# Kernel tuning notes

Measured on AMD Instinct MI355X. Metric: run time of the kernel, lower is better.

Reference implementation:

```python
import jax, jax.numpy as jnp
import numpy as np

INPUT_DIM = 6
HIDDEN = 256
NUM_CLASSES = 8
B = 16
V = 32768


def setup_inputs() -> dict:
    key = jax.random.key(0)
    ks = jax.random.split(key, 8)
    x = jax.random.normal(ks[0], (B, INPUT_DIM, V), dtype=jnp.float32)
    obj_idx = jax.random.randint(ks[1], (B,), 0, NUM_CLASSES)
    # Stacked per-class expert weights (Conv1d kernel_size=1 == pointwise linear)
    s1 = 1.0 / np.sqrt(INPUT_DIM)
    s2 = 1.0 / np.sqrt(HIDDEN)
    w1 = jax.random.uniform(ks[2], (NUM_CLASSES, HIDDEN, INPUT_DIM), jnp.float32, -s1, s1)
    b1 = jax.random.uniform(ks[3], (NUM_CLASSES, HIDDEN), jnp.float32, -s1, s1)
    w2 = jax.random.uniform(ks[4], (NUM_CLASSES, HIDDEN, HIDDEN), jnp.float32, -s2, s2)
    b2 = jax.random.uniform(ks[5], (NUM_CLASSES, HIDDEN), jnp.float32, -s2, s2)
    w3 = jax.random.uniform(ks[6], (NUM_CLASSES, 1, HIDDEN), jnp.float32, -s2, s2)
    b3 = jax.random.uniform(ks[7], (NUM_CLASSES, 1), jnp.float32, -s2, s2)
    return {"x": x, "obj_idx": obj_idx, "w1": w1, "b1": b1,
            "w2": w2, "b2": b2, "w3": w3, "b3": b3}


def reference(x, obj_idx, w1, b1, w2, b2, w3, b3):
    # Gather each sample's expert weights, then run the fused 3-layer pointwise
    # MLP over all B*V positions in one batched einsum per layer (no Python
    # loop over samples, unlike the original torch code).
    # x: [B, 6, V] -> out: [B, 1, V]
    h = jax.nn.relu(jnp.einsum('boi,biv->bov', w1[obj_idx], x) + b1[obj_idx][:, :, None])
    h = jax.nn.relu(jnp.einsum('boi,biv->bov', w2[obj_idx], h) + b2[obj_idx][:, :, None])
    out = jnp.einsum('boi,biv->bov', w3[obj_idx], h) + b3[obj_idx][:, :, None]
    return out
```

## Files before the change

kernel.cpp:

```cpp
#include <hip/hip_runtime.h>
#include <hip/hip_bf16.h>

typedef __bf16 bf16x8 __attribute__((ext_vector_type(8)));
typedef __bf16 bf16x4 __attribute__((ext_vector_type(4)));
typedef float  f32x4  __attribute__((ext_vector_type(4)));

#define V_TOTAL 32768
#define NT      512
#define NV      32
#define NBLK    256

#define W2_LDS  114688
#define H1_LDS  32768
#define RED_LDS 4096
#define LDS_TOT (W2_LDS + H1_LDS + RED_LDS)

#define GLOAD_LDS16(g, l) __builtin_amdgcn_global_load_lds( \
    (const __attribute__((address_space(1))) void*)(g),     \
    (__attribute__((address_space(3))) void*)(l), 16, 0, 0)

__global__ void w2_to_bf16(const float* __restrict__ w2, __bf16* __restrict__ w2b) {
    int i = blockIdx.x * 256 + threadIdx.x;
    int e = i >> 16, q = i & 65535, c = q >> 3, j = q & 7;
    int kt = c >> 10, mt16 = (c >> 6) & 15, ko = (c >> 4) & 3, row = c & 15;
    w2b[i] = (__bf16)w2[e * 65536 + (mt16 * 16 + row) * 256 + kt * 32 + ko * 8 + j];
}

__global__ __launch_bounds__(NT) void fused_mlp(
    const float* __restrict__ x,  const int* __restrict__ obj,
    const float* __restrict__ w1, const float* __restrict__ b1,
    const float* __restrict__ b2, const float* __restrict__ w3,
    const float* __restrict__ b3, const __bf16* __restrict__ w2b,
    float* __restrict__ out)
{
    extern __shared__ __align__(16) char smem[];
    char*  w2s = smem;
    char*  h1t = smem + W2_LDS;
    float* red = (float*)(smem + W2_LDS + H1_LDS);

    const int t    = threadIdx.x;
    const int lane = t & 63;
    const int wv   = t >> 6;
    const int llo  = lane & 15;
    const int lhi  = lane >> 4;
    const int b    = blockIdx.x >> 4;
    const int g    = blockIdx.x & 15;
    const int e    = __builtin_amdgcn_readfirstlane(obj[b]);
    const __bf16* w2sw = w2b + (size_t)e * 65536;

    #pragma unroll
    for (int it = 0; it < 14; ++it) {
        int c0 = it * NT + wv * 64;
        GLOAD_LDS16(w2sw + c0 * 8 + lane * 8, w2s + c0 * 16);
    }

    bf16x8 aa7[2];
    #pragma unroll
    for (int mt = 0; mt < 2; ++mt) {
        int c = 7168 + (2 * wv + mt) * 64 + lane;
        aa7[mt] = *(const bf16x8*)(w2sw + c * 8);
    }

    const float* w1e = w1 + e * 1536;
    bf16x8 aa1[2];
    f32x4  b1f[2], bv[2], wf[2];
    #pragma unroll
    for (int mt2 = 0; mt2 < 2; ++mt2) {
        const int m0 = (2 * wv + mt2) * 16;
        bf16x8 v = {};
        if (lhi == 0)
            #pragma unroll
            for (int j = 0; j < 6; ++j) v[j] = (__bf16)w1e[(m0 + llo) * 6 + j];
        aa1[mt2] = v;
        b1f[mt2] = *(const f32x4*)(b1 + e * 256 + m0 + lhi * 4);
        bv[mt2]  = *(const f32x4*)(b2 + e * 256 + m0 + lhi * 4);
        wf[mt2]  = *(const f32x4*)(w3 + e * 256 + m0 + lhi * 4);
    }
    const float b3e = b3[e];
    const float* xe = x + (size_t)b * 6 * V_TOTAL;

    bf16x8 xf[4];
    #pragma unroll
    for (int pt = 0; pt < 4; ++pt) {
        bf16x8 v = {};
        #pragma unroll
        for (int i = 0; i < 6; ++i)
            v[i] = (__bf16)xe[i * V_TOTAL + g * (NV * 64) + pt * 16 + llo];
        xf[pt] = v;
    }

    for (int iv = 0; iv < NV; ++iv) {
        const int v0 = (g * NV + iv) * 64;

        #pragma unroll
        for (int mt2 = 0; mt2 < 2; ++mt2) {
            const int o = (2 * wv + mt2) * 2 + (lhi >> 1);
            char* wbase = h1t + (o >> 2) * 4096 + (o & 3) * 256
                              + llo * 16 + (lhi & 1) * 8;
            #pragma unroll
            for (int pt = 0; pt < 4; ++pt) {
                f32x4 h = __builtin_amdgcn_mfma_f32_16x16x32_bf16(
                    aa1[mt2], xf[pt], b1f[mt2], 0, 0, 0);
                bf16x4 pk;
                #pragma unroll
                for (int r = 0; r < 4; ++r) pk[r] = (__bf16)fmaxf(h[r], 0.f);
                *(bf16x4*)(wbase + pt * 1024) = pk;
            }
        }
        if (iv + 1 < NV)
            #pragma unroll
            for (int pt = 0; pt < 4; ++pt) {
                bf16x8 v = {};
                #pragma unroll
                for (int i = 0; i < 6; ++i)
                    v[i] = (__bf16)xe[i * V_TOTAL + v0 + 64 + pt * 16 + llo];
                xf[pt] = v;
            }
        __syncthreads();

        f32x4 acc[2][4];
        #pragma unroll
        for (int mt = 0; mt < 2; ++mt)
            #pragma unroll
            for (int nt = 0; nt < 4; ++nt) acc[mt][nt] = bv[mt];
        const char* abase = w2s + wv * 2048 + lane * 16;
        const char* bbase = h1t + lane * 16;
        __builtin_amdgcn_s_setprio(1);
        #pragma unroll
        for (int kt = 0; kt < 7; ++kt) {
            bf16x8 bb[4];
            #pragma unroll
            for (int nt = 0; nt < 4; ++nt)
                bb[nt] = *(const bf16x8*)(bbase + kt * 4096 + nt * 1024);
            #pragma unroll
            for (int mt = 0; mt < 2; ++mt) {
                const bf16x8 aw = *(const bf16x8*)(abase + kt * 16384 + mt * 1024);
                #pragma unroll
                for (int nt = 0; nt < 4; ++nt)
                    acc[mt][nt] = __builtin_amdgcn_mfma_f32_16x16x32_bf16(
                        aw, bb[nt], acc[mt][nt], 0, 0, 0);
            }
        }
        {
            bf16x8 bb[4];
            #pragma unroll
            for (int nt = 0; nt < 4; ++nt)
                bb[nt] = *(const bf16x8*)(bbase + 7 * 4096 + nt * 1024);
            #pragma unroll
            for (int mt = 0; mt < 2; ++mt)
                #pragma unroll
                for (int nt = 0; nt < 4; ++nt)
                    acc[mt][nt] = __builtin_amdgcn_mfma_f32_16x16x32_bf16(
                        aa7[mt], bb[nt], acc[mt][nt], 0, 0, 0);
        }
        __builtin_amdgcn_s_setprio(0);

        float p[4];
        #pragma unroll
        for (int nt = 0; nt < 4; ++nt) {
            float s = 0.f;
            #pragma unroll
            for (int mt = 0; mt < 2; ++mt)
                #pragma unroll
                for (int j = 0; j < 4; ++j)
                    s = fmaf(wf[mt][j], fmaxf(acc[mt][nt][j], 0.f), s);
            s += __shfl_xor(s, 16, 64);
            s += __shfl_xor(s, 32, 64);
            p[nt] = s;
        }
        float* rp = red + (iv & 1) * 512;
        if (lane < 16)
            #pragma unroll
            for (int nt = 0; nt < 4; ++nt)
                rp[wv * 64 + nt * 16 + lane] = p[nt];
        __syncthreads();
        if (t < 64) {
            float s = b3e;
            #pragma unroll
            for (int w8 = 0; w8 < 8; ++w8) s += rp[w8 * 64 + t];
            out[(size_t)b * V_TOTAL + v0 + t] = s;
        }
    }
}

extern "C" void kernel_launch(void* const* d_in, const int* in_sizes, int n_in,
                              void* d_out, int out_size, void* d_ws, size_t ws_size,
                              hipStream_t stream) {
    const float* x   = (const float*)d_in[0];
    const int*   obj = (const int*)d_in[1];
    const float* w1  = (const float*)d_in[2];
    const float* b1  = (const float*)d_in[3];
    const float* w2  = (const float*)d_in[4];
    const float* b2  = (const float*)d_in[5];
    const float* w3  = (const float*)d_in[6];
    const float* b3  = (const float*)d_in[7];
    float*  out = (float*)d_out;
    __bf16* w2b = (__bf16*)d_ws;

    (void)hipFuncSetAttribute((const void*)fused_mlp,
                              hipFuncAttributeMaxDynamicSharedMemorySize, LDS_TOT);

    w2_to_bf16<<<2048, 256, 0, stream>>>(w2, w2b);
    fused_mlp<<<NBLK, NT, LDS_TOT, stream>>>(x, obj, w1, b1, b2, w3, b3, w2b, out);
}
```

Baseline: 84.16 us.

## Double-buffer hidden activations and merge per-iteration barriers into one

```diff
diff --git a/kernel.cpp b/kernel.cpp
--- a/kernel.cpp
+++ b/kernel.cpp
@@ -10,8 +10,9 @@
 #define NV      32
 #define NBLK    256
 
-#define W2_LDS  114688
-#define H1_LDS  32768
+#define NKLDS   5
+#define W2_LDS  (NKLDS * 16384)
+#define H1_LDS  65536
 #define RED_LDS 4096
 #define LDS_TOT (W2_LDS + H1_LDS + RED_LDS)
 
@@ -49,17 +50,19 @@
     const __bf16* w2sw = w2b + (size_t)e * 65536;
 
     #pragma unroll
-    for (int it = 0; it < 14; ++it) {
+    for (int it = 0; it < 10; ++it) {
         int c0 = it * NT + wv * 64;
         GLOAD_LDS16(w2sw + c0 * 8 + lane * 8, w2s + c0 * 16);
     }
 
-    bf16x8 aa7[2];
+    bf16x8 aar[3][2];
     #pragma unroll
-    for (int mt = 0; mt < 2; ++mt) {
-        int c = 7168 + (2 * wv + mt) * 64 + lane;
-        aa7[mt] = *(const bf16x8*)(w2sw + c * 8);
-    }
+    for (int k2 = 0; k2 < 3; ++k2)
+        #pragma unroll
+        for (int mt = 0; mt < 2; ++mt) {
+            int c = (5 + k2) * 1024 + (2 * wv + mt) * 64 + lane;
+            aar[k2][mt] = *(const bf16x8*)(w2sw + c * 8);
+        }
 
     const float* w1e = w1 + e * 1536;
     bf16x8 aa1[2];
@@ -80,22 +83,21 @@
     const float* xe = x + (size_t)b * 6 * V_TOTAL;
 
     bf16x8 xf[4];
-    #pragma unroll
-    for (int pt = 0; pt < 4; ++pt) {
-        bf16x8 v = {};
-        #pragma unroll
-        for (int i = 0; i < 6; ++i)
-            v[i] = (__bf16)xe[i * V_TOTAL + g * (NV * 64) + pt * 16 + llo];
-        xf[pt] = v;
-    }
-
-    for (int iv = 0; iv < NV; ++iv) {
-        const int v0 = (g * NV + iv) * 64;
-
+    auto load_x = [&](int ic) {
+        #pragma unroll
+        for (int pt = 0; pt < 4; ++pt) {
+            bf16x8 v = {};
+            #pragma unroll
+            for (int i = 0; i < 6; ++i)
+                v[i] = (__bf16)xe[i * V_TOTAL + (g * NV + ic) * 64 + pt * 16 + llo];
+            xf[pt] = v;
+        }
+    };
+    auto do_l1 = [&](int pan) {
         #pragma unroll
         for (int mt2 = 0; mt2 < 2; ++mt2) {
             const int o = (2 * wv + mt2) * 2 + (lhi >> 1);
-            char* wbase = h1t + (o >> 2) * 4096 + (o & 3) * 256
+            char* wbase = h1t + pan * 32768 + (o >> 2) * 4096 + (o & 3) * 256
                               + llo * 16 + (lhi & 1) * 8;
             #pragma unroll
             for (int pt = 0; pt < 4; ++pt) {
@@ -107,16 +109,22 @@
                 *(bf16x4*)(wbase + pt * 1024) = pk;
             }
         }
-        if (iv + 1 < NV)
-            #pragma unroll
-            for (int pt = 0; pt < 4; ++pt) {
-                bf16x8 v = {};
-                #pragma unroll
-                for (int i = 0; i < 6; ++i)
-                    v[i] = (__bf16)xe[i * V_TOTAL + v0 + 64 + pt * 16 + llo];
-                xf[pt] = v;
-            }
+    };
+
+    load_x(0);
+    do_l1(0);
+    load_x(1);
+
+    for (int iv = 0; iv < NV; ++iv) {
         __syncthreads();
+
+        if (iv > 0 && t < 64) {
+            const float* rq = red + ((iv - 1) & 1) * 512;
+            float s = b3e;
+            #pragma unroll
+            for (int w8 = 0; w8 < 8; ++w8) s += rq[w8 * 64 + t];
+            out[(size_t)b * V_TOTAL + (g * NV + iv - 1) * 64 + t] = s;
+        }
 
         f32x4 acc[2][4];
         #pragma unroll
@@ -124,10 +132,10 @@
             #pragma unroll
             for (int nt = 0; nt < 4; ++nt) acc[mt][nt] = bv[mt];
         const char* abase = w2s + wv * 2048 + lane * 16;
-        const char* bbase = h1t + lane * 16;
+        const char* bbase = h1t + (iv & 1) * 32768 + lane * 16;
         __builtin_amdgcn_s_setprio(1);
         #pragma unroll
-        for (int kt = 0; kt < 7; ++kt) {
+        for (int kt = 0; kt < 5; ++kt) {
             bf16x8 bb[4];
             #pragma unroll
             for (int nt = 0; nt < 4; ++nt)
@@ -141,17 +149,18 @@
                         aw, bb[nt], acc[mt][nt], 0, 0, 0);
             }
         }
-        {
+        #pragma unroll
+        for (int k2 = 0; k2 < 3; ++k2) {
             bf16x8 bb[4];
             #pragma unroll
             for (int nt = 0; nt < 4; ++nt)
-                bb[nt] = *(const bf16x8*)(bbase + 7 * 4096 + nt * 1024);
+                bb[nt] = *(const bf16x8*)(bbase + (5 + k2) * 4096 + nt * 1024);
             #pragma unroll
             for (int mt = 0; mt < 2; ++mt)
                 #pragma unroll
                 for (int nt = 0; nt < 4; ++nt)
                     acc[mt][nt] = __builtin_amdgcn_mfma_f32_16x16x32_bf16(
-                        aa7[mt], bb[nt], acc[mt][nt], 0, 0, 0);
+                        aar[k2][mt], bb[nt], acc[mt][nt], 0, 0, 0);
         }
         __builtin_amdgcn_s_setprio(0);
 
@@ -173,13 +182,19 @@
             #pragma unroll
             for (int nt = 0; nt < 4; ++nt)
                 rp[wv * 64 + nt * 16 + lane] = p[nt];
-        __syncthreads();
-        if (t < 64) {
-            float s = b3e;
-            #pragma unroll
-            for (int w8 = 0; w8 < 8; ++w8) s += rp[w8 * 64 + t];
-            out[(size_t)b * V_TOTAL + v0 + t] = s;
-        }
+
+        if (iv + 1 < NV) {
+            do_l1((iv + 1) & 1);
+            if (iv + 2 < NV) load_x(iv + 2);
+        }
+    }
+    __syncthreads();
+    if (t < 64) {
+        const float* rq = red + ((NV - 1) & 1) * 512;
+        float s = b3e;
+        #pragma unroll
+        for (int w8 = 0; w8 < 8; ++w8) s += rq[w8 * 64 + t];
+        out[(size_t)b * V_TOTAL + (g * NV + NV - 1) * 64 + t] = s;
     }
 }
 
```

Measured after the change: 81.69 us. 1.03x faster.
